# Optimization experiments

Measured on AMD Instinct MI355X. Metric: run time of the kernel, lower is better.

Reference implementation:

```python
import jax, jax.numpy as jnp
import numpy as np

K = 3       # kernel_size
STRIDE = 1


def setup_inputs() -> dict:
    key = jax.random.key(0)
    k1, k2, k3 = jax.random.split(key, 3)
    B, C, H, W = 128, 64, 32, 32
    O = 64
    OH = (H - K) // STRIDE + 1  # 30
    OW = (W - K) // STRIDE + 1  # 30
    x = jax.random.normal(k1, (B, C, H, W), dtype=jnp.float32)
    weight = jax.random.normal(k2, (O, C, OH, OW, K, K), dtype=jnp.float32)
    bias = jax.random.normal(k3, (O, OH, OW), dtype=jnp.float32)
    return {"x": x, "weight": weight, "bias": bias}


def reference(x, weight, bias):
    # x: [B, C, H, W]; weight: [O, C, OH, OW, K, K]; bias: [O, OH, OW]
    O, C, OH, OW, _, _ = weight.shape
    # Extract all k x k patches in one pass: [B, C*K*K, OH, OW],
    # feature axis ordered (C, kh, kw) with spatial fastest.
    patches = jax.lax.conv_general_dilated_patches(
        x, filter_shape=(K, K), window_strides=(STRIDE, STRIDE), padding="VALID"
    )
    # Faithful to torch einsum 'bcih,coih->bo': the region's channel axis is
    # contracted against the weight's FIRST axis (nominal out_channels), and the
    # output channel is the weight's SECOND axis (requires C == O).
    # Rearrange weight -> [C*K*K (contract), O (output), OH, OW].
    w = jnp.transpose(weight, (0, 4, 5, 1, 2, 3)).reshape(C * K * K, O, OH, OW)
    out = jnp.einsum("bpij,poij->boij", patches, w) + bias[None]
    return out  # [B, O, OH, OW]
```

## Files before the change

kernel.cpp:

```cpp
#include <hip/hip_runtime.h>


typedef __bf16 bf16x8 __attribute__((ext_vector_type(8)));
typedef float f32x4 __attribute__((ext_vector_type(4)));
typedef unsigned long long u64;
typedef unsigned int u32t;
typedef unsigned short u16t;

struct __attribute__((packed, aligned(8))) uf4 { f32x4 v; };

__device__ __forceinline__ u16t f2bf(float f) {
  union { float f; u32t u; } v; v.f = f;
  u32t r = v.u + 0x7fffu + ((v.u >> 16) & 1u);
  return (u16t)(r >> 16);
}
__device__ __forceinline__ u32t pk2(float a, float b) {
  return (u32t)f2bf(a) | ((u32t)f2bf(b) << 16);
}
__device__ __forceinline__ bf16x8 mk_af(u64 lo, u64 hi) {
  union { u64 q[2]; bf16x8 v; } u;
  u.q[0] = lo; u.q[1] = hi;
  return u.v;
}


__global__ __launch_bounds__(256, 2) void lcl_kernel(
    const float* __restrict__ x, const float* __restrict__ wgt,
    const float* __restrict__ bias, float* __restrict__ out) {
  int blk = blockIdx.x;
  int xcd = blk & 7, sg = blk >> 3;
  int t = xcd * 56 + (xcd < 2 ? xcd : 2) + sg;
  int i = t / 15;
  int j0 = (t % 15) * 2;
  int ij0 = i * 30 + j0;

  __shared__ __align__(16) u16t Bt[2 * 2 * 64 * 104];

  const int tid  = threadIdx.x;
  const int wave = tid >> 6;
  const int lane = tid & 63;
  const int lrow = lane & 15;
  const int q    = lane >> 4;

  {
    u64* zp = (u64*)Bt;
#pragma unroll
    for (int k = 0; k < 26; ++k) zp[tid + k * 256] = 0ull;
  }

  int xoffF[3][2];
#pragma unroll
  for (int s = 0; s < 3; ++s)
#pragma unroll
    for (int tt = 0; tt < 2; ++tt) {
      int g = s * 8 + q * 2 + tt, cc = g / 3, kh = g - cc * 3;
      xoffF[s][tt] = cc * 1024 + kh * 32;
    }
  const float* xb0 = x + (wave * 32 + lrow) * 65536 + i * 32 + j0;
  const float* xb1 = xb0 + 16 * 65536;

  const int o_w = tid & 63;
  const float* wb0 = wgt + (size_t)wave * 518400 + o_w * 8100 + ij0 * 9;
  const float* wb1 = wb0 + (size_t)4 * 518400;

  f32x4 av[2][3][2];
  f32x4 wv[2][5];

#define LOAD_CHUNK(C0)                                                        \
  {                                                                           \
    const float* xc0 = xb0 + (C0) * 1024;                                     \
    const float* xc1 = xb1 + (C0) * 1024;                                     \
    _Pragma("unroll") for (int s = 0; s < 3; ++s)                             \
    _Pragma("unroll") for (int tt = 0; tt < 2; ++tt) {                        \
      av[0][s][tt] = ((const uf4*)(xc0 + xoffF[s][tt]))->v;                   \
      av[1][s][tt] = ((const uf4*)(xc1 + xoffF[s][tt]))->v;                   \
    }                                                                         \
    const float* w0 = wb0 + (size_t)(C0) * 518400;                            \
    const float* w1 = wb1 + (size_t)(C0) * 518400;                            \
    _Pragma("unroll") for (int e = 0; e < 4; ++e) {                           \
      wv[0][e] = ((const uf4*)(w0 + e * 4))->v;                               \
      wv[1][e] = ((const uf4*)(w1 + e * 4))->v;                               \
    }                                                                         \
    wv[0][4] = ((const uf4*)(w0 + 14))->v;                                    \
    wv[1][4] = ((const uf4*)(w1 + 14))->v;                                    \
  }

  f32x4 acc[2][2][4];
#pragma unroll
  for (int a = 0; a < 2; ++a)
#pragma unroll
    for (int b = 0; b < 2; ++b)
#pragma unroll
      for (int c = 0; c < 4; ++c) acc[a][b][c] = f32x4{0.f, 0.f, 0.f, 0.f};

  LOAD_CHUNK(0)

  for (int chunk = 0; chunk < 8; ++chunk) {
    u16t* B = Bt + (chunk & 1) * 13312;

#pragma unroll
    for (int p = 0; p < 2; ++p) {
      int ccl = wave + 4 * p;
      u16t* Bp = B + o_w * 104 + ccl * 12;
      *(u32t*)&Bp[0] = pk2(wv[p][0][0], wv[p][0][1]);
      Bp[2]  = f2bf(wv[p][0][2]);
      Bp[4]  = f2bf(wv[p][0][3]);
      Bp[5]  = f2bf(wv[p][1][0]);
      Bp[6]  = f2bf(wv[p][1][1]);
      *(u32t*)&Bp[8] = pk2(wv[p][1][2], wv[p][1][3]);
      Bp[10] = f2bf(wv[p][2][0]);
      u16t* Bq = Bp + 6656;
      *(u32t*)&Bq[0] = pk2(wv[p][2][1], wv[p][2][2]);
      Bq[2]  = f2bf(wv[p][2][3]);
      Bq[4]  = f2bf(wv[p][3][0]);
      Bq[5]  = f2bf(wv[p][3][1]);
      Bq[6]  = f2bf(wv[p][3][2]);
      *(u32t*)&Bq[8] = pk2(wv[p][3][3], wv[p][4][2]);
      Bq[10] = f2bf(wv[p][4][3]);
    }

    u64 rb[2][3][2];
#pragma unroll
    for (int mt = 0; mt < 2; ++mt)
#pragma unroll
      for (int s = 0; s < 3; ++s)
#pragma unroll
        for (int tt = 0; tt < 2; ++tt) {
          const f32x4 vv = av[mt][s][tt];
          rb[mt][s][tt] =
              (u64)pk2(vv[0], vv[1]) | ((u64)pk2(vv[2], vv[3]) << 32);
        }

    __syncthreads();

    if (chunk < 7) LOAD_CHUNK((chunk + 1) * 8)

#pragma unroll
    for (int s = 0; s < 3; ++s) {
      bf16x8 bfr[2][4];
#pragma unroll
      for (int jj = 0; jj < 2; ++jj)
#pragma unroll
        for (int nt = 0; nt < 4; ++nt)
          bfr[jj][nt] = *reinterpret_cast<const bf16x8*>(
              &B[jj * 6656 + (nt * 16 + lrow) * 104 + s * 32 + q * 8]);
#pragma unroll
      for (int mt = 0; mt < 2; ++mt)
#pragma unroll
        for (int jj = 0; jj < 2; ++jj) {
          u64 lo = rb[mt][s][0] >> (jj * 16);
          u64 hi = rb[mt][s][1] >> (jj * 16);
          bf16x8 af = mk_af(lo, hi);
#pragma unroll
          for (int nt = 0; nt < 4; ++nt)
            acc[mt][jj][nt] = __builtin_amdgcn_mfma_f32_16x16x32_bf16(
                af, bfr[jj][nt], acc[mt][jj][nt], 0, 0, 0);
        }
    }
  }

#pragma unroll
  for (int nt = 0; nt < 4; ++nt) {
    int o = nt * 16 + lrow;
    float2 bv = *(const float2*)(bias + o * 900 + ij0);
#pragma unroll
    for (int mt = 0; mt < 2; ++mt) {
#pragma unroll
      for (int r = 0; r < 4; ++r) {
        int b = wave * 32 + mt * 16 + q * 4 + r;
        float2 res;
        res.x = acc[mt][0][nt][r] + bv.x;
        res.y = acc[mt][1][nt][r] + bv.y;
        *(float2*)(out + b * 57600 + o * 900 + ij0) = res;
      }
    }
  }
}

extern "C" void kernel_launch(void* const* d_in, const int* in_sizes, int n_in,
                              void* d_out, int out_size, void* d_ws,
                              size_t ws_size, hipStream_t stream) {
  const float* x    = (const float*)d_in[0];
  const float* wgt  = (const float*)d_in[1];
  const float* bias = (const float*)d_in[2];
  float* out        = (float*)d_out;
  lcl_kernel<<<dim3(450), dim3(256), 0, stream>>>(x, wgt, bias, out);
}
```

Before: 314.1 us.

## Pre-convert input to bf16 in a transposed layout and retile the main kernel

Adds a pre-pass kernel that converts x to bf16 into the workspace, laid out as [c][h][b][w]. A retiled main kernel then reads that copy; each block covers 64 batches, 32 output channels and 6 output columns, giving 600 blocks instead of 450. The new tiling loads each weight row as a contiguous run of 54 floats and reuses the shifted bf16 input rows across the 6 columns. This cuts x reload traffic and in-loop conversion work, at the cost of an extra launch, a 16 MB workspace write/read, and more registers per thread. The old kernel stays as a fallback when no workspace is available.

Result: slower. 322.0 us (+2.5%).

```diff
diff --git a/kernel.cpp b/kernel.cpp
--- a/kernel.cpp
+++ b/kernel.cpp
@@ -8,6 +8,9 @@
 typedef unsigned short u16t;
 
 struct __attribute__((packed, aligned(8))) uf4 { f32x4 v; };
+struct __attribute__((packed, aligned(8))) uf2 { float2 v; };
+struct __attribute__((packed, aligned(4))) uq2 { u64 x, y; };
+struct __attribute__((aligned(16))) ull2 { u64 x, y; };
 
 __device__ __forceinline__ u16t f2bf(float f) {
   union { float f; u32t u; } v; v.f = f;
@@ -17,6 +20,9 @@
 __device__ __forceinline__ u32t pk2(float a, float b) {
   return (u32t)f2bf(a) | ((u32t)f2bf(b) << 16);
 }
+__device__ __forceinline__ u64 pk3(float a, float b, float c) {
+  return (u64)f2bf(a) | ((u64)f2bf(b) << 16) | ((u64)f2bf(c) << 32);
+}
 __device__ __forceinline__ bf16x8 mk_af(u64 lo, u64 hi) {
   union { u64 q[2]; bf16x8 v; } u;
   u.q[0] = lo; u.q[1] = hi;
@@ -24,7 +30,161 @@
 }
 
 
-__global__ __launch_bounds__(256, 2) void lcl_kernel(
+__global__ __launch_bounds__(256) void lcl_prep_x(const float* __restrict__ x,
+                                                  u16t* __restrict__ Xb) {
+  int gid = blockIdx.x * 256 + threadIdx.x;
+  int b  = gid & 127;
+  int ch = gid >> 7;
+  const float* src = x + (size_t)b * 65536 + ch * 32;
+  u16t* dst = Xb + (size_t)gid * 32;
+  u64 qv[8];
+#pragma unroll
+  for (int s = 0; s < 8; ++s) {
+    f32x4 a = ((const uf4*)(src + s * 4))->v;
+    qv[s] = (u64)pk2(a[0], a[1]) | ((u64)pk2(a[2], a[3]) << 32);
+  }
+#pragma unroll
+  for (int s = 0; s < 4; ++s) {
+    ull2 w; w.x = qv[2 * s]; w.y = qv[2 * s + 1];
+    *(ull2*)(dst + s * 8) = w;
+  }
+}
+
+__global__ __launch_bounds__(256, 2) void lcl_main(
+    const u16t* __restrict__ Xb, const float* __restrict__ wgt,
+    const float* __restrict__ bias, float* __restrict__ out) {
+  int bid = blockIdx.x;
+  int xcd = bid & 7, sg = bid >> 3;
+  int t = xcd * 75 + sg;
+  int jg = t % 5;
+  int r  = t / 5;
+  int bg = r & 1, og = (r >> 1) & 1, i = r >> 2;
+  int j0 = jg * 6;
+  int ij0 = i * 30 + j0;
+
+  __shared__ __align__(16) u16t Bt[2 * 6 * 32 * 104];
+
+  const int tid  = threadIdx.x;
+  const int wave = tid >> 6;
+  const int lane = tid & 63;
+  const int lrow = lane & 15;
+  const int q    = lane >> 4;
+
+  const int b_x = bg * 64 + wave * 16 + lrow;
+  const char* xbase = (const char*)Xb;
+  u32t xoff[3][2];
+#pragma unroll
+  for (int s = 0; s < 3; ++s)
+#pragma unroll
+    for (int tt = 0; tt < 2; ++tt) {
+      int g = s * 8 + q * 2 + tt, cc = g / 3, kh = g - cc * 3;
+      xoff[s][tt] = (u32t)(((cc * 32 + (i + kh)) * 128 + b_x) * 64 + j0 * 2);
+    }
+
+  const int ccw = tid >> 5, ow = tid & 31;
+  const float* wb = wgt + ((size_t)ccw * 64 + og * 32 + ow) * 8100 + ij0 * 9;
+
+  uq2   rq[3][2];
+  f32x4 wv[13];
+  float2 wv2;
+
+#define GF(K) ((K) < 52 ? wv[(K) >> 2][(K)&3] : ((K) == 52 ? wv2.x : wv2.y))
+
+#define LOAD_CHUNK(C0)                                                      \
+  {                                                                         \
+    const size_t xadv = (size_t)(C0) * 262144;                              \
+    _Pragma("unroll") for (int s = 0; s < 3; ++s)                           \
+    _Pragma("unroll") for (int tt = 0; tt < 2; ++tt)                        \
+      rq[s][tt] = *(const uq2*)(xbase + xadv + xoff[s][tt]);                \
+    const float* wq = wb + (size_t)(C0) * 518400;                           \
+    _Pragma("unroll") for (int e = 0; e < 13; ++e)                          \
+      wv[e] = ((const uf4*)(wq + e * 4))->v;                                \
+    wv2 = ((const uf2*)(wq + 52))->v;                                       \
+  }
+
+  f32x4 acc[6][2];
+#pragma unroll
+  for (int a = 0; a < 6; ++a)
+#pragma unroll
+    for (int n = 0; n < 2; ++n) acc[a][n] = f32x4{0.f, 0.f, 0.f, 0.f};
+
+  LOAD_CHUNK(0)
+
+  for (int chunk = 0; chunk < 8; ++chunk) {
+    u16t* B = Bt + (chunk & 1) * 19968;
+
+#pragma unroll
+    for (int dj = 0; dj < 6; ++dj) {
+      u16t* Bp = B + dj * 3328 + ow * 104 + ccw * 12;
+#pragma unroll
+      for (int kh = 0; kh < 3; ++kh) {
+        const int k0 = dj * 9 + kh * 3;
+        *(u64*)&Bp[kh * 4] = pk3(GF(k0), GF(k0 + 1), GF(k0 + 2));
+      }
+    }
+
+    u64 rb[3][2][2];
+#pragma unroll
+    for (int s = 0; s < 3; ++s)
+#pragma unroll
+      for (int tt = 0; tt < 2; ++tt) {
+        rb[s][tt][0] = rq[s][tt].x;
+        rb[s][tt][1] = rq[s][tt].y;
+      }
+
+    __syncthreads();
+
+    if (chunk < 7) LOAD_CHUNK((chunk + 1) * 8)
+
+#pragma unroll
+    for (int s = 0; s < 3; ++s) {
+#pragma unroll
+      for (int jj = 0; jj < 6; ++jj) {
+        bf16x8 bfr0 = *(const bf16x8*)&B[jj * 3328 + lrow * 104 + s * 32 + q * 8];
+        bf16x8 bfr1 = *(const bf16x8*)&B[jj * 3328 + (16 + lrow) * 104 + s * 32 + q * 8];
+        u64 lo, hi;
+        if (jj == 0) {
+          lo = rb[s][0][0];
+          hi = rb[s][1][0];
+        } else if (jj < 4) {
+          lo = (rb[s][0][0] >> (16 * jj)) | (rb[s][0][1] << (64 - 16 * jj));
+          hi = (rb[s][1][0] >> (16 * jj)) | (rb[s][1][1] << (64 - 16 * jj));
+        } else if (jj == 4) {
+          lo = rb[s][0][1];
+          hi = rb[s][1][1];
+        } else {
+          lo = rb[s][0][1] >> 16;
+          hi = rb[s][1][1] >> 16;
+        }
+        bf16x8 af = mk_af(lo, hi);
+        acc[jj][0] = __builtin_amdgcn_mfma_f32_16x16x32_bf16(af, bfr0, acc[jj][0], 0, 0, 0);
+        acc[jj][1] = __builtin_amdgcn_mfma_f32_16x16x32_bf16(af, bfr1, acc[jj][1], 0, 0, 0);
+      }
+    }
+  }
+
+  const int b0 = bg * 64 + wave * 16 + q * 4;
+#pragma unroll
+  for (int nt = 0; nt < 2; ++nt) {
+    int o = og * 32 + nt * 16 + lrow;
+    const float* bp = bias + o * 900 + ij0;
+    float2 bv0 = ((const uf2*)bp)->v;
+    float2 bv1 = ((const uf2*)(bp + 2))->v;
+    float2 bv2 = ((const uf2*)(bp + 4))->v;
+#pragma unroll
+    for (int rr = 0; rr < 4; ++rr) {
+      float* op = out + (size_t)(b0 + rr) * 57600 + o * 900 + ij0;
+      float2 r0{acc[0][nt][rr] + bv0.x, acc[1][nt][rr] + bv0.y};
+      float2 r1{acc[2][nt][rr] + bv1.x, acc[3][nt][rr] + bv1.y};
+      float2 r2{acc[4][nt][rr] + bv2.x, acc[5][nt][rr] + bv2.y};
+      ((uf2*)op)->v = r0;
+      ((uf2*)(op + 2))->v = r1;
+      ((uf2*)(op + 4))->v = r2;
+    }
+  }
+}
+
+__global__ __launch_bounds__(256, 2) void lcl_r4(
     const float* __restrict__ x, const float* __restrict__ wgt,
     const float* __restrict__ bias, float* __restrict__ out) {
   int blk = blockIdx.x;
@@ -66,7 +226,7 @@
   f32x4 av[2][3][2];
   f32x4 wv[2][5];
 
-#define LOAD_CHUNK(C0)                                                        \
+#define LOAD_CHUNK4(C0)                                                       \
   {                                                                           \
     const float* xc0 = xb0 + (C0) * 1024;                                     \
     const float* xc1 = xb1 + (C0) * 1024;                                     \
@@ -93,11 +253,10 @@
 #pragma unroll
       for (int c = 0; c < 4; ++c) acc[a][b][c] = f32x4{0.f, 0.f, 0.f, 0.f};
 
-  LOAD_CHUNK(0)
+  LOAD_CHUNK4(0)
 
   for (int chunk = 0; chunk < 8; ++chunk) {
     u16t* B = Bt + (chunk & 1) * 13312;
-
 #pragma unroll
     for (int p = 0; p < 2; ++p) {
       int ccl = wave + 4 * p;
@@ -127,13 +286,12 @@
 #pragma unroll
         for (int tt = 0; tt < 2; ++tt) {
           const f32x4 vv = av[mt][s][tt];
-          rb[mt][s][tt] =
-              (u64)pk2(vv[0], vv[1]) | ((u64)pk2(vv[2], vv[3]) << 32);
+          rb[mt][s][tt] = (u64)pk2(vv[0], vv[1]) | ((u64)pk2(vv[2], vv[3]) << 32);
         }
 
     __syncthreads();
 
-    if (chunk < 7) LOAD_CHUNK((chunk + 1) * 8)
+    if (chunk < 7) LOAD_CHUNK4((chunk + 1) * 8)
 
 #pragma unroll
     for (int s = 0; s < 3; ++s) {
@@ -166,11 +324,11 @@
 #pragma unroll
     for (int mt = 0; mt < 2; ++mt) {
 #pragma unroll
-      for (int r = 0; r < 4; ++r) {
-        int b = wave * 32 + mt * 16 + q * 4 + r;
+      for (int rr = 0; rr < 4; ++rr) {
+        int b = wave * 32 + mt * 16 + q * 4 + rr;
         float2 res;
-        res.x = acc[mt][0][nt][r] + bv.x;
-        res.y = acc[mt][1][nt][r] + bv.y;
+        res.x = acc[mt][0][nt][rr] + bv.x;
+        res.y = acc[mt][1][nt][rr] + bv.y;
         *(float2*)(out + b * 57600 + o * 900 + ij0) = res;
       }
     }
@@ -184,5 +342,10 @@
   const float* wgt  = (const float*)d_in[1];
   const float* bias = (const float*)d_in[2];
   float* out        = (float*)d_out;
-  lcl_kernel<<<dim3(450), dim3(256), 0, stream>>>(x, wgt, bias, out);
-}
+  if (ws_size >= (size_t)16777216 && d_ws != nullptr) {
+    lcl_prep_x<<<dim3(1024), dim3(256), 0, stream>>>(x, (u16t*)d_ws);
+    lcl_main<<<dim3(600), dim3(256), 0, stream>>>((const u16t*)d_ws, wgt, bias, out);
+  } else {
+    lcl_r4<<<dim3(450), dim3(256), 0, stream>>>(x, wgt, bias, out);
+  }
+}
```
